# Kernel optimization log

Measured on AMD Instinct MI355X. Metric: run time of the kernel, lower is better.

The kernel has to match this reference:

```python
import jax, jax.numpy as jnp
import numpy as np

NUM_GRAPHS = 128


def _gcn_conv(x, W, b, src, dst, norm, n_nodes):
    # PyG GCNConv: linear transform, then symmetric-normalized scatter-add aggregation
    h = x @ W                                  # [N, out]
    msg = norm[:, None] * h[src]               # [E+N, out] gathered messages
    out = jax.ops.segment_sum(msg, dst, num_segments=n_nodes)
    return out + b


def setup_inputs() -> dict:
    key = jax.random.key(0)
    ks = jax.random.split(key, 12)
    N, E, H, GE, C = 100000, 1000000, 64, 64, 5
    x = jax.random.normal(ks[0], (N, 2), dtype=jnp.float32)
    edge_index = jax.random.randint(ks[1], (2, E), 0, N, dtype=jnp.int32)
    batch = jnp.sort(jax.random.randint(ks[2], (N,), 0, NUM_GRAPHS, dtype=jnp.int32))
    graph_embedding = jax.random.normal(ks[3], (NUM_GRAPHS, GE), dtype=jnp.float32)
    s = lambda k, shape, fan: jax.random.normal(k, shape, dtype=jnp.float32) * (1.0 / np.sqrt(fan))
    W1 = s(ks[4], (2, H), 2); b1 = jnp.zeros((H,), jnp.float32)
    W2 = s(ks[5], (H, H), H); b2 = jnp.zeros((H,), jnp.float32)
    W3 = s(ks[6], (H, H), H); b3 = jnp.zeros((H,), jnp.float32)
    Wl = s(ks[7], (H + GE, C), H + GE); bl = jnp.zeros((C,), jnp.float32)
    return {"x": x, "edge_index": edge_index, "batch": batch,
            "graph_embedding": graph_embedding,
            "W1": W1, "b1": b1, "W2": W2, "b2": b2, "W3": W3, "b3": b3,
            "Wl": Wl, "bl": bl}


def reference(x, edge_index, batch, graph_embedding, W1, b1, W2, b2, W3, b3, Wl, bl):
    N = x.shape[0]
    loops = jnp.arange(N, dtype=edge_index.dtype)
    src = jnp.concatenate([edge_index[0], loops])   # add self-loops
    dst = jnp.concatenate([edge_index[1], loops])
    deg = jax.ops.segment_sum(jnp.ones_like(dst, dtype=x.dtype), dst, num_segments=N)
    dinv = jnp.where(deg > 0, jax.lax.rsqrt(deg), 0.0)
    norm = dinv[src] * dinv[dst]                    # [E+N]

    h = jax.nn.relu(_gcn_conv(x, W1, b1, src, dst, norm, N))
    h = jax.nn.relu(_gcn_conv(h, W2, b2, src, dst, norm, N))
    h = _gcn_conv(h, W3, b3, src, dst, norm, N)

    # global mean pool over graphs
    sums = jax.ops.segment_sum(h, batch, num_segments=NUM_GRAPHS)
    cnts = jax.ops.segment_sum(jnp.ones((N,), x.dtype), batch, num_segments=NUM_GRAPHS)
    pooled = sums / jnp.maximum(cnts, 1.0)[:, None]

    z = jnp.concatenate([pooled, graph_embedding], axis=1) @ Wl + bl
    return jax.nn.log_softmax(z, axis=1)
```

## Files before the change

### kernel.cpp

```cpp
#include <hip/hip_runtime.h>
#include <hip/hip_bf16.h>
#include <math.h>

#define NG 128
#define CHUNKB 4096
#define NBIN 512
#define EWIN 256

typedef __attribute__((ext_vector_type(8))) short short8;
typedef __attribute__((ext_vector_type(4))) float float4v;

static __device__ __forceinline__ float bf2f(__hip_bfloat16 v) { return __bfloat162float(v); }

__global__ void k_bin_hist(const int* __restrict__ dst, int* __restrict__ hist,
                           int e, int nb) {
    __shared__ int h[NBIN];
    for (int i = threadIdx.x; i < NBIN; i += 256) h[i] = 0;
    __syncthreads();
    int base = blockIdx.x * CHUNKB;
    int lim = e - base; if (lim > CHUNKB) lim = CHUNKB;
    for (int k = threadIdx.x; k < lim; k += 256)
        atomicAdd(&h[dst[base + k] >> 8], 1);
    __syncthreads();
    for (int b = threadIdx.x; b < NBIN; b += 256) hist[b * nb + blockIdx.x] = h[b];
}

__global__ void __launch_bounds__(512) genscan1(int* __restrict__ a, int* __restrict__ bsums, int n) {
    __shared__ int s[512];
    int tid = threadIdx.x;
    int i = blockIdx.x * 512 + tid;
    int v = (i < n) ? a[i] : 0;
    s[tid] = v;
    __syncthreads();
    for (int d = 1; d < 512; d <<= 1) {
        int t = (tid >= d) ? s[tid - d] : 0;
        __syncthreads();
        s[tid] += t;
        __syncthreads();
    }
    if (i < n) a[i] = s[tid] - v;
    if (tid == 511) bsums[blockIdx.x] = s[511];
}

__global__ void __launch_bounds__(512) genscan2(int* __restrict__ bsums, int nb) {
    __shared__ int s[512];
    int tid = threadIdx.x;
    int v = (tid < nb) ? bsums[tid] : 0;
    s[tid] = v;
    __syncthreads();
    for (int d = 1; d < 512; d <<= 1) {
        int t = (tid >= d) ? s[tid - d] : 0;
        __syncthreads();
        s[tid] += t;
        __syncthreads();
    }
    if (tid < nb) bsums[tid] = s[tid] - v;
}

__global__ void k_bin_scatter(const int* __restrict__ srcs, const int* __restrict__ dsts,
                              const int* __restrict__ offsets, const int* __restrict__ bsums,
                              int2* __restrict__ outbuf, int e, int nb) {
    __shared__ int hcnt[NBIN];
    __shared__ int lstart[NBIN];
    __shared__ int ss[256];
    __shared__ int2 stage[CHUNKB];
    int tid = threadIdx.x, blk = blockIdx.x, base = blk * CHUNKB;
    int lim = e - base; if (lim > CHUNKB) lim = CHUNKB;
    for (int i = tid; i < NBIN; i += 256) hcnt[i] = 0;
    __syncthreads();
    for (int k = tid; k < lim; k += 256)
        atomicAdd(&hcnt[dsts[base + k] >> 8], 1);
    __syncthreads();
    int c0 = hcnt[2 * tid], c1 = hcnt[2 * tid + 1];
    int sum = c0 + c1;
    ss[tid] = sum;
    __syncthreads();
    for (int d = 1; d < 256; d <<= 1) {
        int t = (tid >= d) ? ss[tid - d] : 0;
        __syncthreads();
        ss[tid] += t;
        __syncthreads();
    }
    int excl = ss[tid] - sum;
    lstart[2 * tid] = excl;
    lstart[2 * tid + 1] = excl + c0;
    __syncthreads();
    hcnt[2 * tid] = excl;
    hcnt[2 * tid + 1] = excl + c0;
    __syncthreads();
    for (int k = tid; k < lim; k += 256) {
        int2 ed = make_int2(srcs[base + k], dsts[base + k]);
        int p = atomicAdd(&hcnt[ed.y >> 8], 1);
        stage[p] = ed;
    }
    __syncthreads();
    for (int i = tid; i < NBIN; i += 256) {
        int gi = i * nb + blk;
        lstart[i] = offsets[gi] + bsums[gi >> 9] - lstart[i];
    }
    __syncthreads();
    for (int p = tid; p < lim; p += 256) {
        int2 ed = stage[p];
        outbuf[lstart[ed.y >> 8] + p] = ed;
    }
}

__global__ void k_csrA(const int2* __restrict__ ebuck, const int* __restrict__ offsets,
                       const int* __restrict__ bsums, int* __restrict__ row_ptr,
                       float* __restrict__ dinv, int n, int nb, int nbuk, int e_total) {
    __shared__ int lcnt[256];
    __shared__ int ssc[256];
    int b = blockIdx.x, tid = threadIdx.x, n0 = b << 8;
    lcnt[tid] = 0;
    __syncthreads();
    int i0 = b * nb, i1 = (b + 1) * nb;
    int e0 = offsets[i0] + bsums[i0 >> 9];
    int e1 = offsets[i1] + bsums[i1 >> 9];
    for (int i = e0 + tid; i < e1; i += 256)
        atomicAdd(&lcnt[ebuck[i].y - n0], 1);
    __syncthreads();
    int v = lcnt[tid];
    ssc[tid] = v;
    __syncthreads();
    for (int d = 1; d < 256; d <<= 1) {
        int t = (tid >= d) ? ssc[tid - d] : 0;
        __syncthreads();
        ssc[tid] += t;
        __syncthreads();
    }
    int node = n0 + tid;
    if (node < n) {
        row_ptr[node] = e0 + ssc[tid] - v;
        dinv[node] = rsqrtf((float)v + 1.0f);
        if (node == n - 1) row_ptr[n] = e_total;
    }
}

__global__ void k_csrB(const int2* __restrict__ ebuck, const int* __restrict__ offsets,
                       const int* __restrict__ bsums, const int* __restrict__ row_ptr,
                       const float* __restrict__ dinv, int2* __restrict__ csr, int nb) {
    __shared__ int lcur[256];
    int b = blockIdx.x, tid = threadIdx.x, n0 = b << 8;
    lcur[tid] = 0;
    __syncthreads();
    int i0 = b * nb, i1 = (b + 1) * nb;
    int e0 = offsets[i0] + bsums[i0 >> 9];
    int e1 = offsets[i1] + bsums[i1 >> 9];
    for (int i = e0 + tid; i < e1; i += 256) {
        int2 ed = ebuck[i];
        int r = atomicAdd(&lcur[ed.y - n0], 1);
        int pos = row_ptr[ed.y] + r;
        float w = dinv[ed.x] * dinv[ed.y];
        csr[pos] = make_int2(ed.x, __float_as_int(w));
    }
}

__global__ void k_layer1(const int* __restrict__ row_ptr, const int2* __restrict__ edges,
                         const float* __restrict__ x, const float* __restrict__ dinv,
                         const float* __restrict__ W1, const float* __restrict__ b1,
                         __hip_bfloat16* __restrict__ h, int n) {
    __shared__ float w1s[128];
    __shared__ float b1s[64];
    if (threadIdx.x < 128) w1s[threadIdx.x] = W1[threadIdx.x];
    if (threadIdx.x < 64) b1s[threadIdx.x] = b1[threadIdx.x];
    __syncthreads();
    int i = blockIdx.x * blockDim.x + threadIdx.x;
    if (i >= n) return;
    const float2* x2 = (const float2*)x;
    float dd = dinv[i], d2 = dd * dd;
    float2 xi = x2[i];
    float a0 = d2 * xi.x, a1 = d2 * xi.y;
    int lo = row_ptr[i], hi = row_ptr[i + 1];
    int k = lo;
    for (; k + 4 <= hi; k += 4) {
        int2 e0 = edges[k], e1 = edges[k + 1], e2 = edges[k + 2], e3 = edges[k + 3];
        float2 v0 = x2[e0.x], v1 = x2[e1.x], v2 = x2[e2.x], v3 = x2[e3.x];
        a0 += __int_as_float(e0.y) * v0.x; a1 += __int_as_float(e0.y) * v0.y;
        a0 += __int_as_float(e1.y) * v1.x; a1 += __int_as_float(e1.y) * v1.y;
        a0 += __int_as_float(e2.y) * v2.x; a1 += __int_as_float(e2.y) * v2.y;
        a0 += __int_as_float(e3.y) * v3.x; a1 += __int_as_float(e3.y) * v3.y;
    }
    for (; k < hi; k++) {
        int2 e = edges[k];
        float2 v = x2[e.x];
        a0 += __int_as_float(e.y) * v.x;
        a1 += __int_as_float(e.y) * v.y;
    }
    short8* hv = reinterpret_cast<short8*>(h + (size_t)i * 64);
    #pragma unroll
    for (int g = 0; g < 8; g++) {
        short8 pack;
        #pragma unroll
        for (int j = 0; j < 8; j++) {
            int col = g * 8 + j;
            float v = fmaxf(a0 * w1s[col] + a1 * w1s[64 + col] + b1s[col], 0.0f);
            __hip_bfloat16 bv = __float2bfloat16(v);
            pack[j] = *reinterpret_cast<short*>(&bv);
        }
        hv[g] = pack;
    }
}

template <bool FAST>
static __device__ __forceinline__ void agg_node(int lo, int hi, int half, int col,
        const int2* __restrict__ gE, const int2* EW, int wave_lo,
        const uint* __restrict__ hinu, float& ax, float& ay) {
    for (int k = lo; k < hi; k += 16) {
        int ss[8]; float ww[8];
        #pragma unroll
        for (int j = 0; j < 8; j++) {
            int idx = k + 2 * j + half;
            int cidx = idx < hi ? idx : lo;
            int2 ee = FAST ? EW[cidx - wave_lo] : gE[cidx];
            ss[j] = ee.x;
            ww[j] = idx < hi ? __int_as_float(ee.y) : 0.0f;
        }
        uint vv[8];
        #pragma unroll
        for (int j = 0; j < 8; j++) vv[j] = hinu[(size_t)ss[j] * 32 + col];
        #pragma unroll
        for (int j = 0; j < 8; j++) {
            ax += ww[j] * __int_as_float(vv[j] << 16);
            ay += ww[j] * __int_as_float(vv[j] & 0xffff0000u);
        }
    }
}

template <int RELU, int POOL>
__global__ void __launch_bounds__(64, 8) k_aggLin(const int* __restrict__ row_ptr,
                                                  const int2* __restrict__ edges,
                                                  const __hip_bfloat16* __restrict__ hin,
                                                  const float* __restrict__ dinv,
                                                  const __hip_bfloat16* __restrict__ Wf,
                                                  const float* __restrict__ b,
                                                  __hip_bfloat16* __restrict__ hout,
                                                  const int* __restrict__ batch,
                                                  float* __restrict__ sums, int n) {
    __shared__ __attribute__((aligned(16))) __hip_bfloat16 T[16 * 72];
    __shared__ int2 EW[EWIN];
    int lane = threadIdx.x;
    int nb0 = blockIdx.x * 16;
    if (nb0 >= n) return;
    int half = lane >> 5, col = lane & 31;
    const uint* hinu = reinterpret_cast<const uint*>(hin);

    int bidx = nb0 + (lane < 16 ? lane : 16);
    if (bidx > n) bidx = n;
    int rp = row_ptr[bidx];
    int wave_lo = __shfl(rp, 0);
    int wave_hi = __shfl(rp, 16);
    int cnt = wave_hi - wave_lo;
    bool fast = (cnt <= EWIN);
    if (fast)
        for (int i = lane; i < cnt; i += 64) EW[i] = edges[wave_lo + i];

    for (int nn = 0; nn < 16; nn++) {
        int node = nb0 + nn;
        float ax = 0.0f, ay = 0.0f;
        if (node < n) {
            if (half == 0) {
                float dn = dinv[node];
                uint hv = hinu[(size_t)node * 32 + col];
                float dn2 = dn * dn;
                ax = dn2 * __int_as_float(hv << 16);
                ay = dn2 * __int_as_float(hv & 0xffff0000u);
            }
            int lo = __shfl(rp, nn), hi = __shfl(rp, nn + 1);
            if (fast) agg_node<true >(lo, hi, half, col, edges, EW, wave_lo, hinu, ax, ay);
            else      agg_node<false>(lo, hi, half, col, edges, EW, wave_lo, hinu, ax, ay);
        }
        ax += __shfl_xor(ax, 32);
        ay += __shfl_xor(ay, 32);
        if (half == 0) {
            __hip_bfloat16 bx = __float2bfloat16(ax);
            __hip_bfloat16 by = __float2bfloat16(ay);
            uint pack = (uint)(*reinterpret_cast<unsigned short*>(&bx)) |
                        ((uint)(*reinterpret_cast<unsigned short*>(&by)) << 16);
            *reinterpret_cast<uint*>(&T[nn * 72 + 2 * col]) = pack;
        }
    }

    int m = lane & 15, q = lane >> 4;
    short8 a0 = *reinterpret_cast<const short8*>(&T[m * 72 + q * 8]);
    short8 a1 = *reinterpret_cast<const short8*>(&T[m * 72 + 32 + q * 8]);
    int lastn = nb0 + 15 < n ? nb0 + 15 : n - 1;
    bool onegraph = POOL && (nb0 + 15 < n) && (batch[nb0] == batch[lastn]);
    int gA = POOL ? batch[nb0] : 0;
    #pragma unroll
    for (int jt = 0; jt < 4; jt++) {
        short8 bf0 = *reinterpret_cast<const short8*>(Wf + ((size_t)(jt * 2 + 0) * 64 + lane) * 8);
        short8 bf1 = *reinterpret_cast<const short8*>(Wf + ((size_t)(jt * 2 + 1) * 64 + lane) * 8);
        float4v d = {0.0f, 0.0f, 0.0f, 0.0f};
        d = __builtin_amdgcn_mfma_f32_16x16x32_bf16(a0, bf0, d, 0, 0, 0);
        d = __builtin_amdgcn_mfma_f32_16x16x32_bf16(a1, bf1, d, 0, 0, 0);
        float bias = b[jt * 16 + m];
        if (POOL) {
            if (onegraph) {
                float s = (d[0] + bias) + (d[1] + bias) + (d[2] + bias) + (d[3] + bias);
                s += __shfl_xor(s, 16);
                s += __shfl_xor(s, 32);
                if (q == 0) atomicAdd(&sums[gA * 64 + jt * 16 + m], s);
            } else {
                #pragma unroll
                for (int r = 0; r < 4; r++) {
                    int node = nb0 + q * 4 + r;
                    if (node < n)
                        atomicAdd(&sums[batch[node] * 64 + jt * 16 + m], d[r] + bias);
                }
            }
        } else {
            #pragma unroll
            for (int r = 0; r < 4; r++) {
                int node = nb0 + q * 4 + r;
                if (node < n) {
                    float v = d[r] + bias;
                    if (RELU) v = fmaxf(v, 0.0f);
                    hout[(size_t)node * 64 + jt * 16 + m] = __float2bfloat16(v);
                }
            }
        }
    }
}

__global__ void k_prepW(const float* __restrict__ W2, const float* __restrict__ W3,
                        __hip_bfloat16* __restrict__ Wf2, __hip_bfloat16* __restrict__ Wf3) {
    const float* W = blockIdx.x ? W3 : W2;
    __hip_bfloat16* Wf = blockIdx.x ? Wf3 : Wf2;
    int t = threadIdx.x;
    int c = t >> 6, l = t & 63;
    int jt = c >> 1, half = c & 1, nn = l & 15, q = l >> 4;
    #pragma unroll
    for (int j = 0; j < 8; j++) {
        int k = half * 32 + q * 8 + j;
        Wf[t * 8 + j] = __float2bfloat16(W[k * 64 + jt * 16 + nn]);
    }
}

__device__ inline int lower_bound_i(const int* __restrict__ a, int n, int key) {
    int lo = 0, hi = n;
    while (lo < hi) {
        int mid = (lo + hi) >> 1;
        if (a[mid] < key) lo = mid + 1; else hi = mid;
    }
    return lo;
}

__global__ void k_head(const float* __restrict__ sums, const int* __restrict__ batch,
                       const float* __restrict__ ge, const float* __restrict__ Wl,
                       const float* __restrict__ bl, float* __restrict__ out,
                       int n, int ng) {
    int g = blockIdx.x * blockDim.x + threadIdx.x;
    if (g < ng) {
        int lo = lower_bound_i(batch, n, g);
        int hi = lower_bound_i(batch, n, g + 1);
        float c = fmaxf((float)(hi - lo), 1.0f);
        float z[5];
        for (int cl = 0; cl < 5; cl++) z[cl] = bl[cl];
        for (int k = 0; k < 64; k++) {
            float p = sums[g * 64 + k] / c;
            for (int cl = 0; cl < 5; cl++) z[cl] += p * Wl[k * 5 + cl];
        }
        for (int k = 0; k < 64; k++) {
            float p = ge[g * 64 + k];
            for (int cl = 0; cl < 5; cl++) z[cl] += p * Wl[(64 + k) * 5 + cl];
        }
        float m = z[0];
        for (int cl = 1; cl < 5; cl++) m = fmaxf(m, z[cl]);
        float s = 0.0f;
        for (int cl = 0; cl < 5; cl++) s += expf(z[cl] - m);
        float lse = m + logf(s);
        for (int cl = 0; cl < 5; cl++) out[g * 5 + cl] = z[cl] - lse;
    }
}

#define ALIGN16(x) (((x) + 15) & ~(size_t)15)

extern "C" void kernel_launch(void* const* d_in, const int* in_sizes, int n_in,
                              void* d_out, int out_size, void* d_ws, size_t ws_size,
                              hipStream_t stream) {
    const float* x    = (const float*)d_in[0];
    const int*   ei   = (const int*)d_in[1];
    const int*   batch= (const int*)d_in[2];
    const float* ge   = (const float*)d_in[3];
    const float* W1   = (const float*)d_in[4];
    const float* b1   = (const float*)d_in[5];
    const float* W2   = (const float*)d_in[6];
    const float* b2   = (const float*)d_in[7];
    const float* W3   = (const float*)d_in[8];
    const float* b3   = (const float*)d_in[9];
    const float* Wl   = (const float*)d_in[10];
    const float* bl   = (const float*)d_in[11];
    float* out = (float*)d_out;

    const int N = in_sizes[0] / 2;
    const int E = in_sizes[1] / 2;
    const int* src = ei;
    const int* dst = ei + E;
    const int NBUK = (N + 255) >> 8;
    const int nbC  = (E + CHUNKB - 1) / CHUNKB;

    char* wsb = (char*)d_ws;
    float* dinv   = (float*)wsb;                wsb += ALIGN16((size_t)N * 4);
    __hip_bfloat16* h16 = (__hip_bfloat16*)wsb;  wsb += ALIGN16((size_t)64 * N * 2);
    __hip_bfloat16* buf2= (__hip_bfloat16*)wsb;  wsb += ALIGN16((size_t)64 * N * 2);
    float* sums   = (float*)wsb;                wsb += ALIGN16((size_t)NG * 64 * 4);
    __hip_bfloat16* Wf2 = (__hip_bfloat16*)wsb; wsb += ALIGN16((size_t)4096 * 2);
    __hip_bfloat16* Wf3 = (__hip_bfloat16*)wsb; wsb += ALIGN16((size_t)4096 * 2);
    int2*  ebuck  = (int2*)wsb;                 wsb += ALIGN16((size_t)E * 8);
    int2*  csr    = (int2*)wsb;                 wsb += ALIGN16((size_t)E * 8);
    int*   row_ptr= (int*)wsb;                  wsb += ALIGN16((size_t)(N + 1) * 4);
    int*   hist   = (int*)wsb;                  wsb += ALIGN16((size_t)NBIN * nbC * 4);
    int*   bsums  = (int*)wsb;                  wsb += 512 * 4;

    const int BS = 256;
    int gN   = (N + BS - 1) / BS;
    int gF   = (N + 15) / 16;
    int nH   = NBIN * nbC;
    int gH   = (nH + 511) / 512;

    hipMemsetAsync(sums, 0, (size_t)NG * 64 * 4, stream);
    k_bin_hist<<<nbC, BS, 0, stream>>>(dst, hist, E, nbC);
    genscan1<<<gH, 512, 0, stream>>>(hist, bsums, nH);
    genscan2<<<1, 512, 0, stream>>>(bsums, gH);
    k_bin_scatter<<<nbC, BS, 0, stream>>>(src, dst, hist, bsums, ebuck, E, nbC);
    k_csrA<<<NBUK, BS, 0, stream>>>(ebuck, hist, bsums, row_ptr, dinv, N, nbC, NBUK, E);
    k_csrB<<<NBUK, BS, 0, stream>>>(ebuck, hist, bsums, row_ptr, dinv, csr, nbC);
    k_prepW<<<2, 512, 0, stream>>>(W2, W3, Wf2, Wf3);

    k_layer1<<<gN, BS, 0, stream>>>(row_ptr, csr, x, dinv, W1, b1, h16, N);

    k_aggLin<1, 0><<<gF, 64, 0, stream>>>(row_ptr, csr, h16, dinv, Wf2, b2, buf2,
                                          nullptr, nullptr, N);

    k_aggLin<0, 1><<<gF, 64, 0, stream>>>(row_ptr, csr, buf2, dinv, Wf3, b3, nullptr,
                                          batch, sums, N);

    k_head<<<1, 128, 0, stream>>>(sums, batch, ge, Wl, bl, out, N, NG);
}
```

Measured before the change: 232.7 us.

## Fuse CSR build kernels, store source-only CSR, fold normalization into aggregation

```diff
diff --git a/kernel.cpp b/kernel.cpp
--- a/kernel.cpp
+++ b/kernel.cpp
@@ -13,8 +13,11 @@
 static __device__ __forceinline__ float bf2f(__hip_bfloat16 v) { return __bfloat162float(v); }
 
 __global__ void k_bin_hist(const int* __restrict__ dst, int* __restrict__ hist,
+                           float* __restrict__ sums, int* __restrict__ scanctr,
                            int e, int nb) {
     __shared__ int h[NBIN];
+    if (blockIdx.x < 32) sums[blockIdx.x * 256 + threadIdx.x] = 0.0f;
+    if (blockIdx.x == 32 && threadIdx.x == 0) *scanctr = 0;
     for (int i = threadIdx.x; i < NBIN; i += 256) h[i] = 0;
     __syncthreads();
     int base = blockIdx.x * CHUNKB;
@@ -25,8 +28,12 @@
     for (int b = threadIdx.x; b < NBIN; b += 256) hist[b * nb + blockIdx.x] = h[b];
 }
 
-__global__ void __launch_bounds__(512) genscan1(int* __restrict__ a, int* __restrict__ bsums, int n) {
+__global__ void __launch_bounds__(512) genscan_fused(int* __restrict__ a,
+                                                     int* __restrict__ bsums,
+                                                     int* __restrict__ ctr,
+                                                     int n, int nblk) {
     __shared__ int s[512];
+    __shared__ int isLast;
     int tid = threadIdx.x;
     int i = blockIdx.x * 512 + tid;
     int v = (i < n) ? a[i] : 0;
@@ -39,22 +46,31 @@
         __syncthreads();
     }
     if (i < n) a[i] = s[tid] - v;
-    if (tid == 511) bsums[blockIdx.x] = s[511];
-}
-
-__global__ void __launch_bounds__(512) genscan2(int* __restrict__ bsums, int nb) {
-    __shared__ int s[512];
-    int tid = threadIdx.x;
-    int v = (tid < nb) ? bsums[tid] : 0;
-    s[tid] = v;
-    __syncthreads();
-    for (int d = 1; d < 512; d <<= 1) {
-        int t = (tid >= d) ? s[tid - d] : 0;
-        __syncthreads();
-        s[tid] += t;
-        __syncthreads();
-    }
-    if (tid < nb) bsums[tid] = s[tid] - v;
+    if (tid == 511)
+        __hip_atomic_store(&bsums[blockIdx.x], s[511], __ATOMIC_RELAXED,
+                           __HIP_MEMORY_SCOPE_AGENT);
+    __threadfence();
+    if (tid == 0) {
+        int prev = atomicAdd(ctr, 1);
+        isLast = (prev == nblk - 1);
+    }
+    __syncthreads();
+    if (isLast) {
+        __threadfence();
+        int v2 = (tid < nblk) ? __hip_atomic_load(&bsums[tid], __ATOMIC_RELAXED,
+                                                  __HIP_MEMORY_SCOPE_AGENT) : 0;
+        s[tid] = v2;
+        __syncthreads();
+        for (int d = 1; d < 512; d <<= 1) {
+            int t = (tid >= d) ? s[tid - d] : 0;
+            __syncthreads();
+            s[tid] += t;
+            __syncthreads();
+        }
+        if (tid < nblk)
+            __hip_atomic_store(&bsums[tid], s[tid] - v2, __ATOMIC_RELAXED,
+                               __HIP_MEMORY_SCOPE_AGENT);
+    }
 }
 
 __global__ void k_bin_scatter(const int* __restrict__ srcs, const int* __restrict__ dsts,
@@ -105,11 +121,13 @@
     }
 }
 
-__global__ void k_csrA(const int2* __restrict__ ebuck, const int* __restrict__ offsets,
-                       const int* __restrict__ bsums, int* __restrict__ row_ptr,
-                       float* __restrict__ dinv, int n, int nb, int nbuk, int e_total) {
+__global__ void k_csrAB(const int2* __restrict__ ebuck, const int* __restrict__ offsets,
+                        const int* __restrict__ bsums, int* __restrict__ row_ptr,
+                        float* __restrict__ dinv, int* __restrict__ csr_src,
+                        int n, int nb, int e_total) {
     __shared__ int lcnt[256];
     __shared__ int ssc[256];
+    __shared__ int lcur[256];
     int b = blockIdx.x, tid = threadIdx.x, n0 = b << 8;
     lcnt[tid] = 0;
     __syncthreads();
@@ -128,37 +146,43 @@
         ssc[tid] += t;
         __syncthreads();
     }
+    int excl = ssc[tid] - v;
+    lcur[tid] = excl;
     int node = n0 + tid;
     if (node < n) {
-        row_ptr[node] = e0 + ssc[tid] - v;
+        row_ptr[node] = e0 + excl;
         dinv[node] = rsqrtf((float)v + 1.0f);
         if (node == n - 1) row_ptr[n] = e_total;
     }
-}
-
-__global__ void k_csrB(const int2* __restrict__ ebuck, const int* __restrict__ offsets,
-                       const int* __restrict__ bsums, const int* __restrict__ row_ptr,
-                       const float* __restrict__ dinv, int2* __restrict__ csr, int nb) {
-    __shared__ int lcur[256];
-    int b = blockIdx.x, tid = threadIdx.x, n0 = b << 8;
-    lcur[tid] = 0;
-    __syncthreads();
-    int i0 = b * nb, i1 = (b + 1) * nb;
-    int e0 = offsets[i0] + bsums[i0 >> 9];
-    int e1 = offsets[i1] + bsums[i1 >> 9];
+    __syncthreads();
     for (int i = e0 + tid; i < e1; i += 256) {
         int2 ed = ebuck[i];
         int r = atomicAdd(&lcur[ed.y - n0], 1);
-        int pos = row_ptr[ed.y] + r;
-        float w = dinv[ed.x] * dinv[ed.y];
-        csr[pos] = make_int2(ed.x, __float_as_int(w));
-    }
-}
-
-__global__ void k_layer1(const int* __restrict__ row_ptr, const int2* __restrict__ edges,
+        csr_src[e0 + r] = ed.x;
+    }
+}
+
+__global__ void k_layer1(const int* __restrict__ row_ptr, const int* __restrict__ csr_src,
                          const float* __restrict__ x, const float* __restrict__ dinv,
                          const float* __restrict__ W1, const float* __restrict__ b1,
+                         const float* __restrict__ W2, const float* __restrict__ W3,
+                         __hip_bfloat16* __restrict__ Wf2, __hip_bfloat16* __restrict__ Wf3,
                          __hip_bfloat16* __restrict__ h, int n) {
+    if (blockIdx.x < 2) {
+        const float* W = blockIdx.x ? W3 : W2;
+        __hip_bfloat16* Wf = blockIdx.x ? Wf3 : Wf2;
+        #pragma unroll
+        for (int rep = 0; rep < 2; rep++) {
+            int t = threadIdx.x + rep * 256;
+            int c = t >> 6, l = t & 63;
+            int jt = c >> 1, half = c & 1, nn2 = l & 15, q = l >> 4;
+            #pragma unroll
+            for (int j = 0; j < 8; j++) {
+                int k = half * 32 + q * 8 + j;
+                Wf[t * 8 + j] = __float2bfloat16(W[k * 64 + jt * 16 + nn2]);
+            }
+        }
+    }
     __shared__ float w1s[128];
     __shared__ float b1s[64];
     if (threadIdx.x < 128) w1s[threadIdx.x] = W1[threadIdx.x];
@@ -167,25 +191,28 @@
     int i = blockIdx.x * blockDim.x + threadIdx.x;
     if (i >= n) return;
     const float2* x2 = (const float2*)x;
-    float dd = dinv[i], d2 = dd * dd;
+    float dd = dinv[i];
     float2 xi = x2[i];
-    float a0 = d2 * xi.x, a1 = d2 * xi.y;
+    float a0 = dd * xi.x, a1 = dd * xi.y;
     int lo = row_ptr[i], hi = row_ptr[i + 1];
     int k = lo;
     for (; k + 4 <= hi; k += 4) {
-        int2 e0 = edges[k], e1 = edges[k + 1], e2 = edges[k + 2], e3 = edges[k + 3];
-        float2 v0 = x2[e0.x], v1 = x2[e1.x], v2 = x2[e2.x], v3 = x2[e3.x];
-        a0 += __int_as_float(e0.y) * v0.x; a1 += __int_as_float(e0.y) * v0.y;
-        a0 += __int_as_float(e1.y) * v1.x; a1 += __int_as_float(e1.y) * v1.y;
-        a0 += __int_as_float(e2.y) * v2.x; a1 += __int_as_float(e2.y) * v2.y;
-        a0 += __int_as_float(e3.y) * v3.x; a1 += __int_as_float(e3.y) * v3.y;
+        int s0 = csr_src[k], s1 = csr_src[k + 1], s2 = csr_src[k + 2], s3 = csr_src[k + 3];
+        float w0 = dinv[s0], w1 = dinv[s1], w2 = dinv[s2], w3 = dinv[s3];
+        float2 v0 = x2[s0], v1 = x2[s1], v2 = x2[s2], v3 = x2[s3];
+        a0 += w0 * v0.x; a1 += w0 * v0.y;
+        a0 += w1 * v1.x; a1 += w1 * v1.y;
+        a0 += w2 * v2.x; a1 += w2 * v2.y;
+        a0 += w3 * v3.x; a1 += w3 * v3.y;
     }
     for (; k < hi; k++) {
-        int2 e = edges[k];
-        float2 v = x2[e.x];
-        a0 += __int_as_float(e.y) * v.x;
-        a1 += __int_as_float(e.y) * v.y;
-    }
+        int s = csr_src[k];
+        float w = dinv[s];
+        float2 v = x2[s];
+        a0 += w * v.x;
+        a1 += w * v.y;
+    }
+    a0 *= dd; a1 *= dd;
     short8* hv = reinterpret_cast<short8*>(h + (size_t)i * 64);
     #pragma unroll
     for (int g = 0; g < 8; g++) {
@@ -203,7 +230,8 @@
 
 template <bool FAST>
 static __device__ __forceinline__ void agg_node(int lo, int hi, int half, int col,
-        const int2* __restrict__ gE, const int2* EW, int wave_lo,
+        const int* __restrict__ gEs, const float* __restrict__ dinv,
+        const int2* EW, int wave_lo,
         const uint* __restrict__ hinu, float& ax, float& ay) {
     for (int k = lo; k < hi; k += 16) {
         int ss[8]; float ww[8];
@@ -211,7 +239,9 @@
         for (int j = 0; j < 8; j++) {
             int idx = k + 2 * j + half;
             int cidx = idx < hi ? idx : lo;
-            int2 ee = FAST ? EW[cidx - wave_lo] : gE[cidx];
+            int2 ee;
+            if (FAST) ee = EW[cidx - wave_lo];
+            else { int s_ = gEs[cidx]; ee = make_int2(s_, __float_as_int(dinv[s_])); }
             ss[j] = ee.x;
             ww[j] = idx < hi ? __int_as_float(ee.y) : 0.0f;
         }
@@ -228,7 +258,7 @@
 
 template <int RELU, int POOL>
 __global__ void __launch_bounds__(64, 8) k_aggLin(const int* __restrict__ row_ptr,
-                                                  const int2* __restrict__ edges,
+                                                  const int* __restrict__ csr_src,
                                                   const __hip_bfloat16* __restrict__ hin,
                                                   const float* __restrict__ dinv,
                                                   const __hip_bfloat16* __restrict__ Wf,
@@ -252,26 +282,29 @@
     int cnt = wave_hi - wave_lo;
     bool fast = (cnt <= EWIN);
     if (fast)
-        for (int i = lane; i < cnt; i += 64) EW[i] = edges[wave_lo + i];
+        for (int i = lane; i < cnt; i += 64) {
+            int s = csr_src[wave_lo + i];
+            EW[i] = make_int2(s, __float_as_int(dinv[s]));
+        }
 
     for (int nn = 0; nn < 16; nn++) {
         int node = nb0 + nn;
-        float ax = 0.0f, ay = 0.0f;
+        float ax = 0.0f, ay = 0.0f, dn = 0.0f;
         if (node < n) {
             if (half == 0) {
-                float dn = dinv[node];
+                dn = dinv[node];
                 uint hv = hinu[(size_t)node * 32 + col];
-                float dn2 = dn * dn;
-                ax = dn2 * __int_as_float(hv << 16);
-                ay = dn2 * __int_as_float(hv & 0xffff0000u);
+                ax = dn * __int_as_float(hv << 16);
+                ay = dn * __int_as_float(hv & 0xffff0000u);
             }
             int lo = __shfl(rp, nn), hi = __shfl(rp, nn + 1);
-            if (fast) agg_node<true >(lo, hi, half, col, edges, EW, wave_lo, hinu, ax, ay);
-            else      agg_node<false>(lo, hi, half, col, edges, EW, wave_lo, hinu, ax, ay);
+            if (fast) agg_node<true >(lo, hi, half, col, csr_src, dinv, EW, wave_lo, hinu, ax, ay);
+            else      agg_node<false>(lo, hi, half, col, csr_src, dinv, EW, wave_lo, hinu, ax, ay);
         }
         ax += __shfl_xor(ax, 32);
         ay += __shfl_xor(ay, 32);
         if (half == 0) {
+            ax *= dn; ay *= dn;
             __hip_bfloat16 bx = __float2bfloat16(ax);
             __hip_bfloat16 by = __float2bfloat16(ay);
             uint pack = (uint)(*reinterpret_cast<unsigned short*>(&bx)) |
@@ -322,20 +355,6 @@
     }
 }
 
-__global__ void k_prepW(const float* __restrict__ W2, const float* __restrict__ W3,
-                        __hip_bfloat16* __restrict__ Wf2, __hip_bfloat16* __restrict__ Wf3) {
-    const float* W = blockIdx.x ? W3 : W2;
-    __hip_bfloat16* Wf = blockIdx.x ? Wf3 : Wf2;
-    int t = threadIdx.x;
-    int c = t >> 6, l = t & 63;
-    int jt = c >> 1, half = c & 1, nn = l & 15, q = l >> 4;
-    #pragma unroll
-    for (int j = 0; j < 8; j++) {
-        int k = half * 32 + q * 8 + j;
-        Wf[t * 8 + j] = __float2bfloat16(W[k * 64 + jt * 16 + nn]);
-    }
-}
-
 __device__ inline int lower_bound_i(const int* __restrict__ a, int n, int key) {
     int lo = 0, hi = n;
     while (lo < hi) {
@@ -407,10 +426,11 @@
     __hip_bfloat16* Wf2 = (__hip_bfloat16*)wsb; wsb += ALIGN16((size_t)4096 * 2);
     __hip_bfloat16* Wf3 = (__hip_bfloat16*)wsb; wsb += ALIGN16((size_t)4096 * 2);
     int2*  ebuck  = (int2*)wsb;                 wsb += ALIGN16((size_t)E * 8);
-    int2*  csr    = (int2*)wsb;                 wsb += ALIGN16((size_t)E * 8);
+    int*   csr_src= (int*)wsb;                  wsb += ALIGN16((size_t)E * 4);
     int*   row_ptr= (int*)wsb;                  wsb += ALIGN16((size_t)(N + 1) * 4);
     int*   hist   = (int*)wsb;                  wsb += ALIGN16((size_t)NBIN * nbC * 4);
     int*   bsums  = (int*)wsb;                  wsb += 512 * 4;
+    int*   scanctr= (int*)wsb;                  wsb += 16;
 
     const int BS = 256;
     int gN   = (N + BS - 1) / BS;
@@ -418,21 +438,18 @@
     int nH   = NBIN * nbC;
     int gH   = (nH + 511) / 512;
 
-    hipMemsetAsync(sums, 0, (size_t)NG * 64 * 4, stream);
-    k_bin_hist<<<nbC, BS, 0, stream>>>(dst, hist, E, nbC);
-    genscan1<<<gH, 512, 0, stream>>>(hist, bsums, nH);
-    genscan2<<<1, 512, 0, stream>>>(bsums, gH);
+    k_bin_hist<<<nbC, BS, 0, stream>>>(dst, hist, sums, scanctr, E, nbC);
+    genscan_fused<<<gH, 512, 0, stream>>>(hist, bsums, scanctr, nH, gH);
     k_bin_scatter<<<nbC, BS, 0, stream>>>(src, dst, hist, bsums, ebuck, E, nbC);
-    k_csrA<<<NBUK, BS, 0, stream>>>(ebuck, hist, bsums, row_ptr, dinv, N, nbC, NBUK, E);
-    k_csrB<<<NBUK, BS, 0, stream>>>(ebuck, hist, bsums, row_ptr, dinv, csr, nbC);
-    k_prepW<<<2, 512, 0, stream>>>(W2, W3, Wf2, Wf3);
-
-    k_layer1<<<gN, BS, 0, stream>>>(row_ptr, csr, x, dinv, W1, b1, h16, N);
-
-    k_aggLin<1, 0><<<gF, 64, 0, stream>>>(row_ptr, csr, h16, dinv, Wf2, b2, buf2,
+    k_csrAB<<<NBUK, BS, 0, stream>>>(ebuck, hist, bsums, row_ptr, dinv, csr_src, N, nbC, E);
+
+    k_layer1<<<gN, BS, 0, stream>>>(row_ptr, csr_src, x, dinv, W1, b1,
+                                    W2, W3, Wf2, Wf3, h16, N);
+
+    k_aggLin<1, 0><<<gF, 64, 0, stream>>>(row_ptr, csr_src, h16, dinv, Wf2, b2, buf2,
                                           nullptr, nullptr, N);
 
-    k_aggLin<0, 1><<<gF, 64, 0, stream>>>(row_ptr, csr, buf2, dinv, Wf3, b3, nullptr,
+    k_aggLin<0, 1><<<gF, 64, 0, stream>>>(row_ptr, csr_src, buf2, dinv, Wf3, b3, nullptr,
                                           batch, sums, N);
 
     k_head<<<1, 128, 0, stream>>>(sums, batch, ge, Wl, bl, out, N, NG);
```

After: 268.4 us. +15.3%, slower.
